# Kernel tuning notes

Hardware: AMD Instinct MI355X
Metric: run time of the kernel (lower is better)

The kernel has to match this reference:

```python
import jax, jax.numpy as jnp
import numpy as np

B, N, C, H = 1, 1024, 384, 12
DK, DV, P, PV = 16, 16, 4, 4  # scalar key/value dims, query/value points
POINT_KEY_DIM = 4

def setup_inputs() -> dict:
    key = jax.random.key(0)
    ks = jax.random.split(key, 12)
    s = 0.02
    x = jax.random.normal(ks[0], (B, N, C), dtype=jnp.float32)
    # random orthonormal frames via QR
    A = jax.random.normal(ks[1], (B, N, 3, 3), dtype=jnp.float32)
    rotations, _ = jnp.linalg.qr(A)
    translations = jax.random.normal(ks[2], (B, N, 3), dtype=jnp.float32) * 10.0
    Wq  = jax.random.normal(ks[3], (C, H * DK), dtype=jnp.float32) * s
    Wk  = jax.random.normal(ks[4], (C, H * DK), dtype=jnp.float32) * s
    Wv  = jax.random.normal(ks[5], (C, H * DV), dtype=jnp.float32) * s
    Wqp = jax.random.normal(ks[6], (C, H * P * 3), dtype=jnp.float32) * s
    Wkp = jax.random.normal(ks[7], (C, H * P * 3), dtype=jnp.float32) * s
    Wvp = jax.random.normal(ks[8], (C, H * PV * 3), dtype=jnp.float32) * s
    Wout = jax.random.normal(ks[9], (H * DV + H * PV, C), dtype=jnp.float32) * s
    bout = jnp.zeros((C,), dtype=jnp.float32)
    return {"x": x, "rotations": rotations, "translations": translations,
            "Wq": Wq, "Wk": Wk, "Wv": Wv, "Wqp": Wqp, "Wkp": Wkp, "Wvp": Wvp,
            "Wout": Wout, "bout": bout}

def reference(x, rotations, translations, Wq, Wk, Wv, Wqp, Wkp, Wvp, Wout, bout):
    b, n, c = x.shape
    h = H
    # scalar q/k/v: (b,n,h,d)
    qs = (x @ Wq).reshape(b, n, h, DK)
    ks_ = (x @ Wk).reshape(b, n, h, DK)
    vs = (x @ Wv).reshape(b, n, h, DV)
    # local points: (b,n,h,p,3)
    qp = (x @ Wqp).reshape(b, n, h, P, 3)
    kp = (x @ Wkp).reshape(b, n, h, P, 3)
    vp = (x @ Wvp).reshape(b, n, h, PV, 3)
    t = translations[:, :, None, None, :]
    # rotate to global frame
    qpg = jnp.einsum('bnij,bnhpj->bnhpi', rotations, qp) + t
    kpg = jnp.einsum('bnij,bnhpj->bnhpi', rotations, kp) + t
    vpg = jnp.einsum('bnij,bnhpj->bnhpi', rotations, vp) + t
    # scalar attention logits (b,h,i,j)
    attn_scalar = jnp.einsum('bihd,bjhd->bhij', qs, ks_)
    # squared distances summed over points and coords, expanded to avoid (n,n,h,p,3) diff tensor
    q2 = (qpg ** 2).sum((-1, -2))          # (b,n,h)
    k2 = (kpg ** 2).sum((-1, -2))          # (b,n,h)
    qk = jnp.einsum('bihpc,bjhpc->bhij', qpg, kpg)
    dist_sq = (q2.transpose(0, 2, 1)[:, :, :, None]
               + k2.transpose(0, 2, 1)[:, :, None, :]
               - 2.0 * qk)                 # (b,h,i,j)
    gamma = np.sqrt(2.0 / (9.0 * POINT_KEY_DIM)).astype(np.float32)
    inv_sqrt_dk = np.float32(1.0 / np.sqrt(DK))
    logits = (attn_scalar - 0.5 * gamma * dist_sq) * inv_sqrt_dk
    w = jax.nn.softmax(logits, axis=-1)    # (b,h,i,j)
    # scalar output: (b,n,h*dv)
    out_scalar = jnp.einsum('bhij,bjhd->bihd', w, vs).reshape(b, n, h * DV)
    # point output in global frame, then back to local frame of residue i
    out_pts_g = jnp.einsum('bhij,bjhpc->bihpc', w, vpg)   # (b,n,h,pv,3)
    centered = out_pts_g - t
    out_pts_local = jnp.einsum('bnji,bnhpj->bnhpi', rotations, centered)
    out_pts_norm = jnp.sqrt((out_pts_local ** 2).sum(-1)).reshape(b, n, h * PV)
    out = jnp.concatenate([out_scalar, out_pts_norm], axis=-1)
    return out @ Wout + bout
```

## Files before the change

kernel.cpp:

```cpp
#include <hip/hip_runtime.h>
#include <math.h>

#define N_TOK 1024
#define C_DIM 384
#define H_NUM 12
#define PCOLS 1024
#define Q0 0
#define K0 192
#define V0 384
#define QP0 576
#define KP0 720
#define VP0 864
#define ATT_W 240
#define COEF 0.11785113019775792f
#define ISD 0.25f
#define CC2 (COEF * ISD)
#define KV_ROWS 60
#define NZ 4

__global__ __launch_bounds__(256) void k_pack(
    const float* __restrict__ Wq, const float* __restrict__ Wk, const float* __restrict__ Wv,
    const float* __restrict__ Wqp, const float* __restrict__ Wkp, const float* __restrict__ Wvp,
    float* __restrict__ Wall)
{
    int t = blockIdx.x * 256 + threadIdx.x;
    int k = t >> 8;
    int col = (t & 255) * 4;
    float4 v;
    if (col < 192)       v = *(const float4*)(Wq  + k * 192 + col);
    else if (col < 384)  v = *(const float4*)(Wk  + k * 192 + col - 192);
    else if (col < 576)  v = *(const float4*)(Wv  + k * 192 + col - 384);
    else if (col < 720)  v = *(const float4*)(Wqp + k * 144 + col - 576);
    else if (col < 864)  v = *(const float4*)(Wkp + k * 144 + col - 720);
    else if (col < 1008) v = *(const float4*)(Wvp + k * 144 + col - 864);
    else                 v = make_float4(0.f, 0.f, 0.f, 0.f);
    *(float4*)(Wall + k * PCOLS + col) = v;
}

__global__ __launch_bounds__(256) void k_proj(
    const float* __restrict__ x, const float* __restrict__ Wall, float* __restrict__ P)
{
    __shared__ float xs[64][17];
    __shared__ float wsh[16][64];
    int tid = threadIdx.x;
    int i0 = blockIdx.x * 64, c0 = blockIdx.y * 64;
    int lr = tid >> 2, lk = (tid & 3) * 4;
    int wr = tid >> 4, wc = (tid & 15) * 4;
    int ty = tid >> 4, tx = tid & 15;

    float4 xa = *(const float4*)(x + (i0 + lr) * C_DIM + lk);
    float4 wa = *(const float4*)(Wall + wr * PCOLS + c0 + wc);
    float acc[4][4] = {};

    for (int it = 0; it < 24; ++it) {
        xs[lr][lk + 0] = xa.x; xs[lr][lk + 1] = xa.y;
        xs[lr][lk + 2] = xa.z; xs[lr][lk + 3] = xa.w;
        *(float4*)&wsh[wr][wc] = wa;
        __syncthreads();
        if (it < 23) {
            xa = *(const float4*)(x + (i0 + lr) * C_DIM + (it + 1) * 16 + lk);
            wa = *(const float4*)(Wall + ((it + 1) * 16 + wr) * PCOLS + c0 + wc);
        }
#pragma unroll
        for (int kk = 0; kk < 16; ++kk) {
            float4 b = *(float4*)&wsh[kk][tx * 4];
            float a0 = xs[ty * 4 + 0][kk];
            float a1 = xs[ty * 4 + 1][kk];
            float a2 = xs[ty * 4 + 2][kk];
            float a3 = xs[ty * 4 + 3][kk];
            acc[0][0] = fmaf(a0, b.x, acc[0][0]); acc[0][1] = fmaf(a0, b.y, acc[0][1]);
            acc[0][2] = fmaf(a0, b.z, acc[0][2]); acc[0][3] = fmaf(a0, b.w, acc[0][3]);
            acc[1][0] = fmaf(a1, b.x, acc[1][0]); acc[1][1] = fmaf(a1, b.y, acc[1][1]);
            acc[1][2] = fmaf(a1, b.z, acc[1][2]); acc[1][3] = fmaf(a1, b.w, acc[1][3]);
            acc[2][0] = fmaf(a2, b.x, acc[2][0]); acc[2][1] = fmaf(a2, b.y, acc[2][1]);
            acc[2][2] = fmaf(a2, b.z, acc[2][2]); acc[2][3] = fmaf(a2, b.w, acc[2][3]);
            acc[3][0] = fmaf(a3, b.x, acc[3][0]); acc[3][1] = fmaf(a3, b.y, acc[3][1]);
            acc[3][2] = fmaf(a3, b.z, acc[3][2]); acc[3][3] = fmaf(a3, b.w, acc[3][3]);
        }
        __syncthreads();
    }
#pragma unroll
    for (int r = 0; r < 4; ++r) {
        *(float4*)(P + (i0 + ty * 4 + r) * PCOLS + c0 + tx * 4) =
            make_float4(acc[r][0], acc[r][1], acc[r][2], acc[r][3]);
    }
}

__global__ __launch_bounds__(256) void k_prep(
    const float* __restrict__ P, const float* __restrict__ rot, const float* __restrict__ trans,
    float* __restrict__ KVg, float* __restrict__ Qg, float* __restrict__ qcg)
{
    __shared__ float kb[29 * 128];
    __shared__ float qb[29 * 128];
    __shared__ float vb[28 * 128];
    __shared__ float qcb[128];
    int h = blockIdx.y, nb = blockIdx.x;
    int tid = threadIdx.x;
    int nl = tid & 127, role = tid >> 7;
    int n = nb * 128 + nl;
    const float* R = rot + n * 9;
    float R00 = R[0], R01 = R[1], R02 = R[2];
    float R10 = R[3], R11 = R[4], R12 = R[5];
    float R20 = R[6], R21 = R[7], R22 = R[8];
    float t0 = trans[n * 3 + 0], t1 = trans[n * 3 + 1], t2 = trans[n * 3 + 2];

    if (role == 0) {
        const float* kr = P + n * PCOLS + K0 + h * 16;
#pragma unroll
        for (int d = 0; d < 16; ++d) kb[d * 128 + nl] = kr[d];
        const float* kp = P + n * PCOLS + KP0 + h * 12;
        float k2 = 0.f;
#pragma unroll
        for (int pt = 0; pt < 4; ++pt) {
            float p0 = kp[pt * 3 + 0], p1 = kp[pt * 3 + 1], p2 = kp[pt * 3 + 2];
            float g0 = R00 * p0 + R01 * p1 + R02 * p2 + t0;
            float g1 = R10 * p0 + R11 * p1 + R12 * p2 + t1;
            float g2 = R20 * p0 + R21 * p1 + R22 * p2 + t2;
            kb[(16 + pt * 3 + 0) * 128 + nl] = g0;
            kb[(16 + pt * 3 + 1) * 128 + nl] = g1;
            kb[(16 + pt * 3 + 2) * 128 + nl] = g2;
            k2 += g0 * g0 + g1 * g1 + g2 * g2;
        }
        kb[28 * 128 + nl] = -CC2 * k2;
    } else {
        const float* qr = P + n * PCOLS + Q0 + h * 16;
#pragma unroll
        for (int d = 0; d < 16; ++d) qb[d * 128 + nl] = qr[d] * ISD;
        const float* qp = P + n * PCOLS + QP0 + h * 12;
        float q2 = 0.f;
#pragma unroll
        for (int pt = 0; pt < 4; ++pt) {
            float p0 = qp[pt * 3 + 0], p1 = qp[pt * 3 + 1], p2 = qp[pt * 3 + 2];
            float g0 = R00 * p0 + R01 * p1 + R02 * p2 + t0;
            float g1 = R10 * p0 + R11 * p1 + R12 * p2 + t1;
            float g2 = R20 * p0 + R21 * p1 + R22 * p2 + t2;
            qb[(16 + pt * 3 + 0) * 128 + nl] = g0 * (2.f * CC2);
            qb[(16 + pt * 3 + 1) * 128 + nl] = g1 * (2.f * CC2);
            qb[(16 + pt * 3 + 2) * 128 + nl] = g2 * (2.f * CC2);
            q2 += g0 * g0 + g1 * g1 + g2 * g2;
        }
        qb[28 * 128 + nl] = 1.0f;
        qcb[nl] = fmaf(-CC2, q2, -4.0f);
        const float* vr = P + n * PCOLS + V0 + h * 16;
#pragma unroll
        for (int d = 0; d < 16; ++d) vb[d * 128 + nl] = vr[d];
        const float* vp = P + n * PCOLS + VP0 + h * 12;
#pragma unroll
        for (int pt = 0; pt < 4; ++pt) {
            float p0 = vp[pt * 3 + 0], p1 = vp[pt * 3 + 1], p2 = vp[pt * 3 + 2];
            vb[(16 + pt * 3 + 0) * 128 + nl] = R00 * p0 + R01 * p1 + R02 * p2 + t0;
            vb[(16 + pt * 3 + 1) * 128 + nl] = R10 * p0 + R11 * p1 + R12 * p2 + t1;
            vb[(16 + pt * 3 + 2) * 128 + nl] = R20 * p0 + R21 * p1 + R22 * p2 + t2;
        }
    }
    __syncthreads();

    for (int u = tid; u < 57 * 32; u += 256) {
        int d = u >> 5, c4 = u & 31;
        float4 v = (d < 29) ? *(float4*)&kb[d * 128 + c4 * 4]
                            : *(float4*)&vb[(d - 29) * 128 + c4 * 4];
        *(float4*)&KVg[(h * KV_ROWS + d) * 1024 + nb * 128 + c4 * 4] = v;
    }
    for (int u = tid; u < 29 * 32; u += 256) {
        int d = u >> 5, c4 = u & 31;
        *(float4*)&Qg[(h * 29 + d) * 1024 + nb * 128 + c4 * 4] = *(float4*)&qb[d * 128 + c4 * 4];
    }
    if (tid < 32) *(float4*)&qcg[h * 1024 + nb * 128 + tid * 4] = *(float4*)&qcb[tid * 4];
}

__global__ __launch_bounds__(256, 3) void k_attn(
    const float* __restrict__ KVg, const float* __restrict__ Qg,
    const float* __restrict__ qcg, float* __restrict__ part)
{
    __shared__ float Qs[29 * 64];
    __shared__ float KV[2][KV_ROWS * 64];
    int tid = threadIdx.x;
    int lane = tid & 63, w = tid >> 6;
    int ty = tid >> 3, tx = tid & 7;

    int bid = blockIdx.x;
    int xcd = bid & 7, slot = bid >> 3;
    int pair = xcd * 6 + (slot >> 4);
    int bx = slot & 15;
    int h = pair % H_NUM;
    int z = pair / H_NUM;

    int i0 = bx * 64;
    int jz0 = z * 256;
    const float* KVh = KVg + h * KV_ROWS * 1024;

    for (int u = tid; u < 29 * 16; u += 256) {
        int d = u >> 4, c4 = u & 15;
        *(float4*)&Qs[d * 64 + c4 * 4] = *(const float4*)&Qg[(h * 29 + d) * 1024 + i0 + c4 * 4];
    }
    float qc[2];
#pragma unroll
    for (int r = 0; r < 2; ++r) qc[r] = qcg[h * 1024 + i0 + ty * 2 + r];

    int nst = (w < 3) ? 4 : 3;
#define STAGE(T) do { float* buf_ = KV[(T) & 1]; int j0_ = jz0 + (T) * 64;        \
        for (int m_ = 0; m_ < nst; ++m_) {                                        \
            int g_ = w * 4 + m_;                                                  \
            const float* src_ = KVh + (g_ * 4 + (lane >> 4)) * 1024 + j0_ + (lane & 15) * 4; \
            float* dst_ = buf_ + g_ * 256;                                        \
            __builtin_amdgcn_global_load_lds(                                     \
                (const __attribute__((address_space(1))) void*)src_,              \
                (__attribute__((address_space(3))) void*)dst_, 16, 0, 0);         \
        } } while (0)

    STAGE(0);
    __syncthreads();

    float out[2][28] = {};
    float denom[2] = {};

    for (int t = 0; t < 4; ++t) {
        if (t < 3) STAGE(t + 1);
        const float* Kb = KV[t & 1];
        const float* Vb = Kb + 29 * 64;

        float s[2][8] = {};
#pragma unroll
        for (int d = 0; d < 29; ++d) {
            float2 qv = *(const float2*)&Qs[d * 64 + ty * 2];
            float4 k0 = *(const float4*)&Kb[d * 64 + tx * 8];
            float4 k1 = *(const float4*)&Kb[d * 64 + tx * 8 + 4];
            float ka[8] = {k0.x, k0.y, k0.z, k0.w, k1.x, k1.y, k1.z, k1.w};
#pragma unroll
            for (int j = 0; j < 8; ++j) {
                s[0][j] = fmaf(qv.x, ka[j], s[0][j]);
                s[1][j] = fmaf(qv.y, ka[j], s[1][j]);
            }
        }

        float p[2][8];
#pragma unroll
        for (int r = 0; r < 2; ++r) {
#pragma unroll
            for (int j = 0; j < 8; ++j) {
                p[r][j] = __expf(s[r][j] + qc[r]);
                denom[r] += p[r][j];
            }
        }

#pragma unroll
        for (int d = 0; d < 28; ++d) {
            float4 v0 = *(const float4*)&Vb[d * 64 + tx * 8];
            float4 v1 = *(const float4*)&Vb[d * 64 + tx * 8 + 4];
            float va[8] = {v0.x, v0.y, v0.z, v0.w, v1.x, v1.y, v1.z, v1.w};
#pragma unroll
            for (int r = 0; r < 2; ++r) {
                float acc = out[r][d];
#pragma unroll
                for (int j = 0; j < 8; ++j) acc = fmaf(p[r][j], va[j], acc);
                out[r][d] = acc;
            }
        }
        __syncthreads();
    }

#pragma unroll
    for (int m = 1; m <= 4; m <<= 1) {
#pragma unroll
        for (int r = 0; r < 2; ++r) {
#pragma unroll
            for (int d = 0; d < 28; ++d) out[r][d] += __shfl_xor(out[r][d], m, 64);
            denom[r] += __shfl_xor(denom[r], m, 64);
        }
    }
    if (tx == 0) {
#pragma unroll
        for (int r = 0; r < 2; ++r) {
#pragma unroll
            for (int d = 0; d < 28; ++d) Qs[d * 64 + ty * 2 + r] = out[r][d];
            Qs[28 * 64 + ty * 2 + r] = denom[r];
        }
    }
    __syncthreads();
    for (int u = tid; u < 29 * 64; u += 256) {
        part[((z * H_NUM + h) * 29 + (u >> 6)) * N_TOK + i0 + (u & 63)] = Qs[u];
    }
}

__global__ __launch_bounds__(256) void k_comb(
    const float* __restrict__ part, const float* __restrict__ rot,
    const float* __restrict__ trans, float* __restrict__ att)
{
    int t = blockIdx.x * 256 + threadIdx.x;
    int h = t >> 10, i = t & 1023;
    float v[29];
#pragma unroll
    for (int c = 0; c < 29; ++c) {
        float s = 0.f;
#pragma unroll
        for (int z = 0; z < NZ; ++z)
            s += part[((z * H_NUM + h) * 29 + c) * N_TOK + i];
        v[c] = s;
    }
    float inv = 1.f / v[28];
    float* arow = att + i * ATT_W;
#pragma unroll
    for (int d = 0; d < 16; ++d) arow[h * 16 + d] = v[d] * inv;
    float t0 = trans[i * 3 + 0], t1 = trans[i * 3 + 1], t2v = trans[i * 3 + 2];
    const float* R = rot + i * 9;
#pragma unroll
    for (int p = 0; p < 4; ++p) {
        float c0 = v[16 + p * 3 + 0] * inv - t0;
        float c1 = v[16 + p * 3 + 1] * inv - t1;
        float c2 = v[16 + p * 3 + 2] * inv - t2v;
        float l0 = R[0] * c0 + R[3] * c1 + R[6] * c2;
        float l1 = R[1] * c0 + R[4] * c1 + R[7] * c2;
        float l2 = R[2] * c0 + R[5] * c1 + R[8] * c2;
        arow[192 + h * 4 + p] = sqrtf(l0 * l0 + l1 * l1 + l2 * l2);
    }
}

__global__ __launch_bounds__(256) void k_out(
    const float* __restrict__ att, const float* __restrict__ Wout,
    const float* __restrict__ bout, float* __restrict__ out)
{
    __shared__ float xs[64][17];
    __shared__ float wsh[16][64];
    int tid = threadIdx.x;
    int i0 = blockIdx.x * 64, c0 = blockIdx.y * 64;
    int lr = tid >> 2, lk = (tid & 3) * 4;
    int wr = tid >> 4, wc = (tid & 15) * 4;
    int ty = tid >> 4, tx = tid & 15;

    float4 xa = *(const float4*)(att + (i0 + lr) * ATT_W + lk);
    float4 wa = *(const float4*)(Wout + wr * C_DIM + c0 + wc);
    float acc[4][4] = {};

    for (int it = 0; it < 15; ++it) {
        xs[lr][lk + 0] = xa.x; xs[lr][lk + 1] = xa.y;
        xs[lr][lk + 2] = xa.z; xs[lr][lk + 3] = xa.w;
        *(float4*)&wsh[wr][wc] = wa;
        __syncthreads();
        if (it < 14) {
            xa = *(const float4*)(att + (i0 + lr) * ATT_W + (it + 1) * 16 + lk);
            wa = *(const float4*)(Wout + ((it + 1) * 16 + wr) * C_DIM + c0 + wc);
        }
#pragma unroll
        for (int kk = 0; kk < 16; ++kk) {
            float4 b = *(float4*)&wsh[kk][tx * 4];
            float a0 = xs[ty * 4 + 0][kk];
            float a1 = xs[ty * 4 + 1][kk];
            float a2 = xs[ty * 4 + 2][kk];
            float a3 = xs[ty * 4 + 3][kk];
            acc[0][0] = fmaf(a0, b.x, acc[0][0]); acc[0][1] = fmaf(a0, b.y, acc[0][1]);
            acc[0][2] = fmaf(a0, b.z, acc[0][2]); acc[0][3] = fmaf(a0, b.w, acc[0][3]);
            acc[1][0] = fmaf(a1, b.x, acc[1][0]); acc[1][1] = fmaf(a1, b.y, acc[1][1]);
            acc[1][2] = fmaf(a1, b.z, acc[1][2]); acc[1][3] = fmaf(a1, b.w, acc[1][3]);
            acc[2][0] = fmaf(a2, b.x, acc[2][0]); acc[2][1] = fmaf(a2, b.y, acc[2][1]);
            acc[2][2] = fmaf(a2, b.z, acc[2][2]); acc[2][3] = fmaf(a2, b.w, acc[2][3]);
            acc[3][0] = fmaf(a3, b.x, acc[3][0]); acc[3][1] = fmaf(a3, b.y, acc[3][1]);
            acc[3][2] = fmaf(a3, b.z, acc[3][2]); acc[3][3] = fmaf(a3, b.w, acc[3][3]);
        }
        __syncthreads();
    }
    float4 bb = *(const float4*)(bout + c0 + tx * 4);
#pragma unroll
    for (int r = 0; r < 4; ++r) {
        *(float4*)(out + (i0 + ty * 4 + r) * C_DIM + c0 + tx * 4) =
            make_float4(acc[r][0] + bb.x, acc[r][1] + bb.y, acc[r][2] + bb.z, acc[r][3] + bb.w);
    }
}

extern "C" void kernel_launch(void* const* d_in, const int* in_sizes, int n_in,
                              void* d_out, int out_size, void* d_ws, size_t ws_size,
                              hipStream_t stream) {
    const float* x     = (const float*)d_in[0];
    const float* rot   = (const float*)d_in[1];
    const float* trans = (const float*)d_in[2];
    const float* Wq    = (const float*)d_in[3];
    const float* Wk    = (const float*)d_in[4];
    const float* Wv    = (const float*)d_in[5];
    const float* Wqp   = (const float*)d_in[6];
    const float* Wkp   = (const float*)d_in[7];
    const float* Wvp   = (const float*)d_in[8];
    const float* Wout  = (const float*)d_in[9];
    const float* bout  = (const float*)d_in[10];
    float* out = (float*)d_out;

    float* ws = (float*)d_ws;
    float* Wall = ws;
    float* P    = Wall + C_DIM * PCOLS;
    float* KVg  = P    + N_TOK * PCOLS;
    float* Qg   = KVg  + H_NUM * KV_ROWS * 1024;
    float* qcg  = Qg   + H_NUM * 29 * 1024;
    float* part = ws;
    float* att  = Qg;

    k_pack<<<384, 256, 0, stream>>>(Wq, Wk, Wv, Wqp, Wkp, Wvp, Wall);
    k_proj<<<dim3(16, 16), 256, 0, stream>>>(x, Wall, P);
    k_prep<<<dim3(8, 12), 256, 0, stream>>>(P, rot, trans, KVg, Qg, qcg);
    k_attn<<<768, 256, 0, stream>>>(KVg, Qg, qcg, part);
    k_comb<<<48, 256, 0, stream>>>(part, rot, trans, att);
    k_out<<<dim3(16, 6), 256, 0, stream>>>(att, Wout, bout, out);
}
```

Before: 94.05 us.

## Replace LDS-tiled projection GEMMs with register-only double-buffered global loads

Both small GEMMs (input projection and output projection) stop staging tiles in shared memory. Each thread now loads its own x/att rows and weight columns straight from global memory into registers, double-buffered so the next slice's loads overlap the current FMAs, and no barriers are needed. The output GEMM also shrinks to 1x4 outputs per thread with four times as many blocks to improve occupancy. The trade-off is losing the shared-memory reuse across the block, so redundant global and L2 traffic rises, and the caches must absorb the repeated weight reads.

```diff
diff --git a/kernel.cpp b/kernel.cpp
--- a/kernel.cpp
+++ b/kernel.cpp
@@ -37,53 +37,55 @@
     *(float4*)(Wall + k * PCOLS + col) = v;
 }
 
-__global__ __launch_bounds__(256) void k_proj(
+__global__ __launch_bounds__(256, 1) void k_proj(
     const float* __restrict__ x, const float* __restrict__ Wall, float* __restrict__ P)
 {
-    __shared__ float xs[64][17];
-    __shared__ float wsh[16][64];
     int tid = threadIdx.x;
-    int i0 = blockIdx.x * 64, c0 = blockIdx.y * 64;
-    int lr = tid >> 2, lk = (tid & 3) * 4;
-    int wr = tid >> 4, wc = (tid & 15) * 4;
     int ty = tid >> 4, tx = tid & 15;
-
-    float4 xa = *(const float4*)(x + (i0 + lr) * C_DIM + lk);
-    float4 wa = *(const float4*)(Wall + wr * PCOLS + c0 + wc);
+    int row0 = blockIdx.x * 64 + ty * 4;
+    int col0 = blockIdx.y * 64 + tx * 4;
+    const float* xr = x + row0 * C_DIM;
+    const float* wp = Wall + col0;
+
     float acc[4][4] = {};
-
-    for (int it = 0; it < 24; ++it) {
-        xs[lr][lk + 0] = xa.x; xs[lr][lk + 1] = xa.y;
-        xs[lr][lk + 2] = xa.z; xs[lr][lk + 3] = xa.w;
-        *(float4*)&wsh[wr][wc] = wa;
-        __syncthreads();
-        if (it < 23) {
-            xa = *(const float4*)(x + (i0 + lr) * C_DIM + (it + 1) * 16 + lk);
-            wa = *(const float4*)(Wall + ((it + 1) * 16 + wr) * PCOLS + c0 + wc);
-        }
-#pragma unroll
-        for (int kk = 0; kk < 16; ++kk) {
-            float4 b = *(float4*)&wsh[kk][tx * 4];
-            float a0 = xs[ty * 4 + 0][kk];
-            float a1 = xs[ty * 4 + 1][kk];
-            float a2 = xs[ty * 4 + 2][kk];
-            float a3 = xs[ty * 4 + 3][kk];
-            acc[0][0] = fmaf(a0, b.x, acc[0][0]); acc[0][1] = fmaf(a0, b.y, acc[0][1]);
-            acc[0][2] = fmaf(a0, b.z, acc[0][2]); acc[0][3] = fmaf(a0, b.w, acc[0][3]);
-            acc[1][0] = fmaf(a1, b.x, acc[1][0]); acc[1][1] = fmaf(a1, b.y, acc[1][1]);
-            acc[1][2] = fmaf(a1, b.z, acc[1][2]); acc[1][3] = fmaf(a1, b.w, acc[1][3]);
-            acc[2][0] = fmaf(a2, b.x, acc[2][0]); acc[2][1] = fmaf(a2, b.y, acc[2][1]);
-            acc[2][2] = fmaf(a2, b.z, acc[2][2]); acc[2][3] = fmaf(a2, b.w, acc[2][3]);
-            acc[3][0] = fmaf(a3, b.x, acc[3][0]); acc[3][1] = fmaf(a3, b.y, acc[3][1]);
-            acc[3][2] = fmaf(a3, b.z, acc[3][2]); acc[3][3] = fmaf(a3, b.w, acc[3][3]);
-        }
-        __syncthreads();
-    }
-#pragma unroll
-    for (int r = 0; r < 4; ++r) {
-        *(float4*)(P + (i0 + ty * 4 + r) * PCOLS + c0 + tx * 4) =
+    float A[4][4], B[4][4], An[4][4], Bn[4][4];
+
+#pragma unroll
+    for (int r = 0; r < 4; ++r) *(float4*)A[r] = *(const float4*)(xr + r * C_DIM);
+#pragma unroll
+    for (int u = 0; u < 4; ++u) *(float4*)B[u] = *(const float4*)(wp + u * PCOLS);
+
+#define PROJ_FMA(AA, BB)                                                      \
+    _Pragma("unroll")                                                         \
+    for (int u = 0; u < 4; ++u) {                                             \
+        _Pragma("unroll")                                                     \
+        for (int r = 0; r < 4; ++r) {                                         \
+            _Pragma("unroll")                                                 \
+            for (int c = 0; c < 4; ++c)                                       \
+                acc[r][c] = fmaf(AA[r][u], BB[u][c], acc[r][c]);              \
+        }                                                                     \
+    }
+
+    for (int q = 0; q < 96; q += 2) {
+        int k1 = (q + 1) * 4;
+#pragma unroll
+        for (int r = 0; r < 4; ++r) *(float4*)An[r] = *(const float4*)(xr + r * C_DIM + k1);
+#pragma unroll
+        for (int u = 0; u < 4; ++u) *(float4*)Bn[u] = *(const float4*)(wp + (k1 + u) * PCOLS);
+        PROJ_FMA(A, B);
+        if (q + 2 < 96) {
+            int k2 = (q + 2) * 4;
+#pragma unroll
+            for (int r = 0; r < 4; ++r) *(float4*)A[r] = *(const float4*)(xr + r * C_DIM + k2);
+#pragma unroll
+            for (int u = 0; u < 4; ++u) *(float4*)B[u] = *(const float4*)(wp + (k2 + u) * PCOLS);
+        }
+        PROJ_FMA(An, Bn);
+    }
+#pragma unroll
+    for (int r = 0; r < 4; ++r)
+        *(float4*)(P + (row0 + r) * PCOLS + col0) =
             make_float4(acc[r][0], acc[r][1], acc[r][2], acc[r][3]);
-    }
 }
 
 __global__ __launch_bounds__(256) void k_prep(
@@ -315,55 +317,49 @@
     }
 }
 
-__global__ __launch_bounds__(256) void k_out(
+__global__ __launch_bounds__(256, 1) void k_out(
     const float* __restrict__ att, const float* __restrict__ Wout,
     const float* __restrict__ bout, float* __restrict__ out)
 {
-    __shared__ float xs[64][17];
-    __shared__ float wsh[16][64];
     int tid = threadIdx.x;
-    int i0 = blockIdx.x * 64, c0 = blockIdx.y * 64;
-    int lr = tid >> 2, lk = (tid & 3) * 4;
-    int wr = tid >> 4, wc = (tid & 15) * 4;
     int ty = tid >> 4, tx = tid & 15;
-
-    float4 xa = *(const float4*)(att + (i0 + lr) * ATT_W + lk);
-    float4 wa = *(const float4*)(Wout + wr * C_DIM + c0 + wc);
-    float acc[4][4] = {};
-
-    for (int it = 0; it < 15; ++it) {
-        xs[lr][lk + 0] = xa.x; xs[lr][lk + 1] = xa.y;
-        xs[lr][lk + 2] = xa.z; xs[lr][lk + 3] = xa.w;
-        *(float4*)&wsh[wr][wc] = wa;
-        __syncthreads();
-        if (it < 14) {
-            xa = *(const float4*)(att + (i0 + lr) * ATT_W + (it + 1) * 16 + lk);
-            wa = *(const float4*)(Wout + ((it + 1) * 16 + wr) * C_DIM + c0 + wc);
-        }
-#pragma unroll
-        for (int kk = 0; kk < 16; ++kk) {
-            float4 b = *(float4*)&wsh[kk][tx * 4];
-            float a0 = xs[ty * 4 + 0][kk];
-            float a1 = xs[ty * 4 + 1][kk];
-            float a2 = xs[ty * 4 + 2][kk];
-            float a3 = xs[ty * 4 + 3][kk];
-            acc[0][0] = fmaf(a0, b.x, acc[0][0]); acc[0][1] = fmaf(a0, b.y, acc[0][1]);
-            acc[0][2] = fmaf(a0, b.z, acc[0][2]); acc[0][3] = fmaf(a0, b.w, acc[0][3]);
-            acc[1][0] = fmaf(a1, b.x, acc[1][0]); acc[1][1] = fmaf(a1, b.y, acc[1][1]);
-            acc[1][2] = fmaf(a1, b.z, acc[1][2]); acc[1][3] = fmaf(a1, b.w, acc[1][3]);
-            acc[2][0] = fmaf(a2, b.x, acc[2][0]); acc[2][1] = fmaf(a2, b.y, acc[2][1]);
-            acc[2][2] = fmaf(a2, b.z, acc[2][2]); acc[2][3] = fmaf(a2, b.w, acc[2][3]);
-            acc[3][0] = fmaf(a3, b.x, acc[3][0]); acc[3][1] = fmaf(a3, b.y, acc[3][1]);
-            acc[3][2] = fmaf(a3, b.z, acc[3][2]); acc[3][3] = fmaf(a3, b.w, acc[3][3]);
-        }
-        __syncthreads();
-    }
-    float4 bb = *(const float4*)(bout + c0 + tx * 4);
-#pragma unroll
-    for (int r = 0; r < 4; ++r) {
-        *(float4*)(out + (i0 + ty * 4 + r) * C_DIM + c0 + tx * 4) =
-            make_float4(acc[r][0] + bb.x, acc[r][1] + bb.y, acc[r][2] + bb.z, acc[r][3] + bb.w);
-    }
+    int row = blockIdx.x * 16 + ty;
+    int col0 = blockIdx.y * 64 + tx * 4;
+    const float* ar = att + row * ATT_W;
+    const float* wp = Wout + col0;
+
+    float acc[4] = {};
+    float A[4], B[4][4], An[4], Bn[4][4];
+
+    *(float4*)A = *(const float4*)ar;
+#pragma unroll
+    for (int u = 0; u < 4; ++u) *(float4*)B[u] = *(const float4*)(wp + u * C_DIM);
+
+#define OUT_FMA(AA, BB)                                                       \
+    _Pragma("unroll")                                                         \
+    for (int u = 0; u < 4; ++u) {                                             \
+        _Pragma("unroll")                                                     \
+        for (int c = 0; c < 4; ++c)                                           \
+            acc[c] = fmaf(AA[u], BB[u][c], acc[c]);                           \
+    }
+
+    for (int q = 0; q < 60; q += 2) {
+        int k1 = (q + 1) * 4;
+        *(float4*)An = *(const float4*)(ar + k1);
+#pragma unroll
+        for (int u = 0; u < 4; ++u) *(float4*)Bn[u] = *(const float4*)(wp + (k1 + u) * C_DIM);
+        OUT_FMA(A, B);
+        if (q + 2 < 60) {
+            int k2 = (q + 2) * 4;
+            *(float4*)A = *(const float4*)(ar + k2);
+#pragma unroll
+            for (int u = 0; u < 4; ++u) *(float4*)B[u] = *(const float4*)(wp + (k2 + u) * C_DIM);
+        }
+        OUT_FMA(An, Bn);
+    }
+    float4 bb = *(const float4*)(bout + col0);
+    *(float4*)(out + row * C_DIM + col0) =
+        make_float4(acc[0] + bb.x, acc[1] + bb.y, acc[2] + bb.z, acc[3] + bb.w);
 }
 
 extern "C" void kernel_launch(void* const* d_in, const int* in_sizes, int n_in,
@@ -396,5 +392,5 @@
     k_prep<<<dim3(8, 12), 256, 0, stream>>>(P, rot, trans, KVg, Qg, qcg);
     k_attn<<<768, 256, 0, stream>>>(KVg, Qg, qcg, part);
     k_comb<<<48, 256, 0, stream>>>(part, rot, trans, att);
-    k_out<<<dim3(16, 6), 256, 0, stream>>>(att, Wout, bout, out);
-}
+    k_out<<<dim3(64, 6), 256, 0, stream>>>(att, Wout, bout, out);
+}
```

Result: slower. 108.2 us (+15.0%).

## Load GEMM A operands directly into registers and double-buffer weight tiles

Applied to the files above, without the earlier changes.

Both the projection and output GEMMs now read their A operands straight from global memory into registers as float4 vectors instead of staging them in shared memory. The weight tile is double-buffered in shared memory, so each iteration needs one barrier instead of two. The output GEMM shrinks to 32-row tiles with 2 rows per thread, doubling the block count to fill more compute units. The cost is more global/L2 traffic for A, since threads sharing rows load them redundantly, and higher register use.

```diff
diff --git a/kernel.cpp b/kernel.cpp
--- a/kernel.cpp
+++ b/kernel.cpp
@@ -40,50 +40,55 @@
 __global__ __launch_bounds__(256) void k_proj(
     const float* __restrict__ x, const float* __restrict__ Wall, float* __restrict__ P)
 {
-    __shared__ float xs[64][17];
-    __shared__ float wsh[16][64];
+    __shared__ float wsh[2][16][64];
     int tid = threadIdx.x;
-    int i0 = blockIdx.x * 64, c0 = blockIdx.y * 64;
-    int lr = tid >> 2, lk = (tid & 3) * 4;
+    int ty = tid >> 4, tx = tid & 15;
     int wr = tid >> 4, wc = (tid & 15) * 4;
-    int ty = tid >> 4, tx = tid & 15;
-
-    float4 xa = *(const float4*)(x + (i0 + lr) * C_DIM + lk);
-    float4 wa = *(const float4*)(Wall + wr * PCOLS + c0 + wc);
+    int row0 = blockIdx.x * 64 + ty * 4;
+    int col0 = blockIdx.y * 64;
+    const float* xr = x + row0 * C_DIM;
+
     float acc[4][4] = {};
+    {
+        float4 w0 = *(const float4*)(Wall + wr * PCOLS + col0 + wc);
+        *(float4*)&wsh[0][wr][wc] = w0;
+    }
+    __syncthreads();
 
     for (int it = 0; it < 24; ++it) {
-        xs[lr][lk + 0] = xa.x; xs[lr][lk + 1] = xa.y;
-        xs[lr][lk + 2] = xa.z; xs[lr][lk + 3] = xa.w;
-        *(float4*)&wsh[wr][wc] = wa;
+        float4 Ar[4][4];
+#pragma unroll
+        for (int r = 0; r < 4; ++r)
+#pragma unroll
+            for (int q = 0; q < 4; ++q)
+                Ar[r][q] = *(const float4*)(xr + r * C_DIM + it * 16 + q * 4);
+        if (it < 23) {
+            float4 wn = *(const float4*)(Wall + ((it + 1) * 16 + wr) * PCOLS + col0 + wc);
+            *(float4*)&wsh[(it + 1) & 1][wr][wc] = wn;
+        }
+        const float (*wb)[64] = wsh[it & 1];
+#pragma unroll
+        for (int q = 0; q < 4; ++q) {
+#pragma unroll
+            for (int u = 0; u < 4; ++u) {
+                float4 b = *(const float4*)&wb[q * 4 + u][tx * 4];
+#pragma unroll
+                for (int r = 0; r < 4; ++r) {
+                    float a = (u == 0) ? Ar[r][q].x : (u == 1) ? Ar[r][q].y
+                             : (u == 2) ? Ar[r][q].z : Ar[r][q].w;
+                    acc[r][0] = fmaf(a, b.x, acc[r][0]);
+                    acc[r][1] = fmaf(a, b.y, acc[r][1]);
+                    acc[r][2] = fmaf(a, b.z, acc[r][2]);
+                    acc[r][3] = fmaf(a, b.w, acc[r][3]);
+                }
+            }
+        }
         __syncthreads();
-        if (it < 23) {
-            xa = *(const float4*)(x + (i0 + lr) * C_DIM + (it + 1) * 16 + lk);
-            wa = *(const float4*)(Wall + ((it + 1) * 16 + wr) * PCOLS + c0 + wc);
-        }
-#pragma unroll
-        for (int kk = 0; kk < 16; ++kk) {
-            float4 b = *(float4*)&wsh[kk][tx * 4];
-            float a0 = xs[ty * 4 + 0][kk];
-            float a1 = xs[ty * 4 + 1][kk];
-            float a2 = xs[ty * 4 + 2][kk];
-            float a3 = xs[ty * 4 + 3][kk];
-            acc[0][0] = fmaf(a0, b.x, acc[0][0]); acc[0][1] = fmaf(a0, b.y, acc[0][1]);
-            acc[0][2] = fmaf(a0, b.z, acc[0][2]); acc[0][3] = fmaf(a0, b.w, acc[0][3]);
-            acc[1][0] = fmaf(a1, b.x, acc[1][0]); acc[1][1] = fmaf(a1, b.y, acc[1][1]);
-            acc[1][2] = fmaf(a1, b.z, acc[1][2]); acc[1][3] = fmaf(a1, b.w, acc[1][3]);
-            acc[2][0] = fmaf(a2, b.x, acc[2][0]); acc[2][1] = fmaf(a2, b.y, acc[2][1]);
-            acc[2][2] = fmaf(a2, b.z, acc[2][2]); acc[2][3] = fmaf(a2, b.w, acc[2][3]);
-            acc[3][0] = fmaf(a3, b.x, acc[3][0]); acc[3][1] = fmaf(a3, b.y, acc[3][1]);
-            acc[3][2] = fmaf(a3, b.z, acc[3][2]); acc[3][3] = fmaf(a3, b.w, acc[3][3]);
-        }
-        __syncthreads();
-    }
-#pragma unroll
-    for (int r = 0; r < 4; ++r) {
-        *(float4*)(P + (i0 + ty * 4 + r) * PCOLS + c0 + tx * 4) =
+    }
+#pragma unroll
+    for (int r = 0; r < 4; ++r)
+        *(float4*)(P + (row0 + r) * PCOLS + col0 + tx * 4) =
             make_float4(acc[r][0], acc[r][1], acc[r][2], acc[r][3]);
-    }
 }
 
 __global__ __launch_bounds__(256) void k_prep(
@@ -319,51 +324,56 @@
     const float* __restrict__ att, const float* __restrict__ Wout,
     const float* __restrict__ bout, float* __restrict__ out)
 {
-    __shared__ float xs[64][17];
-    __shared__ float wsh[16][64];
+    __shared__ float wsh[2][16][64];
     int tid = threadIdx.x;
-    int i0 = blockIdx.x * 64, c0 = blockIdx.y * 64;
-    int lr = tid >> 2, lk = (tid & 3) * 4;
+    int ty = tid >> 4, tx = tid & 15;
     int wr = tid >> 4, wc = (tid & 15) * 4;
-    int ty = tid >> 4, tx = tid & 15;
-
-    float4 xa = *(const float4*)(att + (i0 + lr) * ATT_W + lk);
-    float4 wa = *(const float4*)(Wout + wr * C_DIM + c0 + wc);
-    float acc[4][4] = {};
+    int row0 = blockIdx.x * 32 + ty * 2;
+    int col0 = blockIdx.y * 64;
+    const float* ar = att + row0 * ATT_W;
+
+    float acc[2][4] = {};
+    {
+        float4 w0 = *(const float4*)(Wout + wr * C_DIM + col0 + wc);
+        *(float4*)&wsh[0][wr][wc] = w0;
+    }
+    __syncthreads();
 
     for (int it = 0; it < 15; ++it) {
-        xs[lr][lk + 0] = xa.x; xs[lr][lk + 1] = xa.y;
-        xs[lr][lk + 2] = xa.z; xs[lr][lk + 3] = xa.w;
-        *(float4*)&wsh[wr][wc] = wa;
+        float4 Ar[2][4];
+#pragma unroll
+        for (int r = 0; r < 2; ++r)
+#pragma unroll
+            for (int q = 0; q < 4; ++q)
+                Ar[r][q] = *(const float4*)(ar + r * ATT_W + it * 16 + q * 4);
+        if (it < 14) {
+            float4 wn = *(const float4*)(Wout + ((it + 1) * 16 + wr) * C_DIM + col0 + wc);
+            *(float4*)&wsh[(it + 1) & 1][wr][wc] = wn;
+        }
+        const float (*wb)[64] = wsh[it & 1];
+#pragma unroll
+        for (int q = 0; q < 4; ++q) {
+#pragma unroll
+            for (int u = 0; u < 4; ++u) {
+                float4 b = *(const float4*)&wb[q * 4 + u][tx * 4];
+#pragma unroll
+                for (int r = 0; r < 2; ++r) {
+                    float a = (u == 0) ? Ar[r][q].x : (u == 1) ? Ar[r][q].y
+                             : (u == 2) ? Ar[r][q].z : Ar[r][q].w;
+                    acc[r][0] = fmaf(a, b.x, acc[r][0]);
+                    acc[r][1] = fmaf(a, b.y, acc[r][1]);
+                    acc[r][2] = fmaf(a, b.z, acc[r][2]);
+                    acc[r][3] = fmaf(a, b.w, acc[r][3]);
+                }
+            }
+        }
         __syncthreads();
-        if (it < 14) {
-            xa = *(const float4*)(att + (i0 + lr) * ATT_W + (it + 1) * 16 + lk);
-            wa = *(const float4*)(Wout + ((it + 1) * 16 + wr) * C_DIM + c0 + wc);
-        }
-#pragma unroll
-        for (int kk = 0; kk < 16; ++kk) {
-            float4 b = *(float4*)&wsh[kk][tx * 4];
-            float a0 = xs[ty * 4 + 0][kk];
-            float a1 = xs[ty * 4 + 1][kk];
-            float a2 = xs[ty * 4 + 2][kk];
-            float a3 = xs[ty * 4 + 3][kk];
-            acc[0][0] = fmaf(a0, b.x, acc[0][0]); acc[0][1] = fmaf(a0, b.y, acc[0][1]);
-            acc[0][2] = fmaf(a0, b.z, acc[0][2]); acc[0][3] = fmaf(a0, b.w, acc[0][3]);
-            acc[1][0] = fmaf(a1, b.x, acc[1][0]); acc[1][1] = fmaf(a1, b.y, acc[1][1]);
-            acc[1][2] = fmaf(a1, b.z, acc[1][2]); acc[1][3] = fmaf(a1, b.w, acc[1][3]);
-            acc[2][0] = fmaf(a2, b.x, acc[2][0]); acc[2][1] = fmaf(a2, b.y, acc[2][1]);
-            acc[2][2] = fmaf(a2, b.z, acc[2][2]); acc[2][3] = fmaf(a2, b.w, acc[2][3]);
-            acc[3][0] = fmaf(a3, b.x, acc[3][0]); acc[3][1] = fmaf(a3, b.y, acc[3][1]);
-            acc[3][2] = fmaf(a3, b.z, acc[3][2]); acc[3][3] = fmaf(a3, b.w, acc[3][3]);
-        }
-        __syncthreads();
-    }
-    float4 bb = *(const float4*)(bout + c0 + tx * 4);
-#pragma unroll
-    for (int r = 0; r < 4; ++r) {
-        *(float4*)(out + (i0 + ty * 4 + r) * C_DIM + c0 + tx * 4) =
+    }
+    float4 bb = *(const float4*)(bout + col0 + tx * 4);
+#pragma unroll
+    for (int r = 0; r < 2; ++r)
+        *(float4*)(out + (row0 + r) * C_DIM + col0 + tx * 4) =
             make_float4(acc[r][0] + bb.x, acc[r][1] + bb.y, acc[r][2] + bb.z, acc[r][3] + bb.w);
-    }
 }
 
 extern "C" void kernel_launch(void* const* d_in, const int* in_sizes, int n_in,
@@ -396,5 +406,5 @@
     k_prep<<<dim3(8, 12), 256, 0, stream>>>(P, rot, trans, KVg, Qg, qcg);
     k_attn<<<768, 256, 0, stream>>>(KVg, Qg, qcg, part);
     k_comb<<<48, 256, 0, stream>>>(part, rot, trans, att);
-    k_out<<<dim3(16, 6), 256, 0, stream>>>(att, Wout, bout, out);
-}
+    k_out<<<dim3(32, 6), 256, 0, stream>>>(att, Wout, bout, out);
+}
```

After: 100.2 us. +6.6%, slower.

## Fuse weight packing into projection GEMM and keep attention queries in registers

Applied to the files above, without the earlier changes.

Removes the separate weight-packing kernel: the projection GEMM now reads directly from the six weight matrices, choosing a base pointer per 64-column tile. The x tile in shared memory is transposed so each thread reads four rows with one float4 load. In the attention kernel, each thread's 29x2 query values are held in registers instead of being read from shared memory on every iteration, and the launch-bounds occupancy hint drops from 3 to 2 blocks to make room for the extra registers. Workspace buffers are laid out separately instead of aliasing. This saves a launch and a global round-trip, at the risk of lower occupancy in the attention kernel.

```diff
diff --git a/kernel.cpp b/kernel.cpp
--- a/kernel.cpp
+++ b/kernel.cpp
@@ -18,29 +18,13 @@
 #define KV_ROWS 60
 #define NZ 4
 
-__global__ __launch_bounds__(256) void k_pack(
+__global__ __launch_bounds__(256) void k_proj(
+    const float* __restrict__ x,
     const float* __restrict__ Wq, const float* __restrict__ Wk, const float* __restrict__ Wv,
     const float* __restrict__ Wqp, const float* __restrict__ Wkp, const float* __restrict__ Wvp,
-    float* __restrict__ Wall)
-{
-    int t = blockIdx.x * 256 + threadIdx.x;
-    int k = t >> 8;
-    int col = (t & 255) * 4;
-    float4 v;
-    if (col < 192)       v = *(const float4*)(Wq  + k * 192 + col);
-    else if (col < 384)  v = *(const float4*)(Wk  + k * 192 + col - 192);
-    else if (col < 576)  v = *(const float4*)(Wv  + k * 192 + col - 384);
-    else if (col < 720)  v = *(const float4*)(Wqp + k * 144 + col - 576);
-    else if (col < 864)  v = *(const float4*)(Wkp + k * 144 + col - 720);
-    else if (col < 1008) v = *(const float4*)(Wvp + k * 144 + col - 864);
-    else                 v = make_float4(0.f, 0.f, 0.f, 0.f);
-    *(float4*)(Wall + k * PCOLS + col) = v;
-}
-
-__global__ __launch_bounds__(256) void k_proj(
-    const float* __restrict__ x, const float* __restrict__ Wall, float* __restrict__ P)
-{
-    __shared__ float xs[64][17];
+    float* __restrict__ P)
+{
+    __shared__ float xs[16][68];
     __shared__ float wsh[16][64];
     int tid = threadIdx.x;
     int i0 = blockIdx.x * 64, c0 = blockIdx.y * 64;
@@ -48,42 +32,49 @@
     int wr = tid >> 4, wc = (tid & 15) * 4;
     int ty = tid >> 4, tx = tid & 15;
 
+    int col = c0 + wc;
+    const float* Wb; int od, cb;
+    if (col < 192)       { Wb = Wq;  od = 192; cb = col; }
+    else if (col < 384)  { Wb = Wk;  od = 192; cb = col - 192; }
+    else if (col < 576)  { Wb = Wv;  od = 192; cb = col - 384; }
+    else if (col < 720)  { Wb = Wqp; od = 144; cb = col - 576; }
+    else if (col < 864)  { Wb = Wkp; od = 144; cb = col - 720; }
+    else if (col < 1008) { Wb = Wvp; od = 144; cb = col - 864; }
+    else                 { Wb = nullptr; od = 0; cb = 0; }
+
     float4 xa = *(const float4*)(x + (i0 + lr) * C_DIM + lk);
-    float4 wa = *(const float4*)(Wall + wr * PCOLS + c0 + wc);
+    float4 wa = Wb ? *(const float4*)(Wb + wr * od + cb) : make_float4(0.f, 0.f, 0.f, 0.f);
     float acc[4][4] = {};
 
     for (int it = 0; it < 24; ++it) {
-        xs[lr][lk + 0] = xa.x; xs[lr][lk + 1] = xa.y;
-        xs[lr][lk + 2] = xa.z; xs[lr][lk + 3] = xa.w;
+        xs[lk + 0][lr] = xa.x; xs[lk + 1][lr] = xa.y;
+        xs[lk + 2][lr] = xa.z; xs[lk + 3][lr] = xa.w;
         *(float4*)&wsh[wr][wc] = wa;
         __syncthreads();
         if (it < 23) {
             xa = *(const float4*)(x + (i0 + lr) * C_DIM + (it + 1) * 16 + lk);
-            wa = *(const float4*)(Wall + ((it + 1) * 16 + wr) * PCOLS + c0 + wc);
+            wa = Wb ? *(const float4*)(Wb + ((it + 1) * 16 + wr) * od + cb)
+                    : make_float4(0.f, 0.f, 0.f, 0.f);
         }
 #pragma unroll
         for (int kk = 0; kk < 16; ++kk) {
+            float4 a = *(float4*)&xs[kk][ty * 4];
             float4 b = *(float4*)&wsh[kk][tx * 4];
-            float a0 = xs[ty * 4 + 0][kk];
-            float a1 = xs[ty * 4 + 1][kk];
-            float a2 = xs[ty * 4 + 2][kk];
-            float a3 = xs[ty * 4 + 3][kk];
-            acc[0][0] = fmaf(a0, b.x, acc[0][0]); acc[0][1] = fmaf(a0, b.y, acc[0][1]);
-            acc[0][2] = fmaf(a0, b.z, acc[0][2]); acc[0][3] = fmaf(a0, b.w, acc[0][3]);
-            acc[1][0] = fmaf(a1, b.x, acc[1][0]); acc[1][1] = fmaf(a1, b.y, acc[1][1]);
-            acc[1][2] = fmaf(a1, b.z, acc[1][2]); acc[1][3] = fmaf(a1, b.w, acc[1][3]);
-            acc[2][0] = fmaf(a2, b.x, acc[2][0]); acc[2][1] = fmaf(a2, b.y, acc[2][1]);
-            acc[2][2] = fmaf(a2, b.z, acc[2][2]); acc[2][3] = fmaf(a2, b.w, acc[2][3]);
-            acc[3][0] = fmaf(a3, b.x, acc[3][0]); acc[3][1] = fmaf(a3, b.y, acc[3][1]);
-            acc[3][2] = fmaf(a3, b.z, acc[3][2]); acc[3][3] = fmaf(a3, b.w, acc[3][3]);
-        }
-        __syncthreads();
-    }
-#pragma unroll
-    for (int r = 0; r < 4; ++r) {
+            acc[0][0] = fmaf(a.x, b.x, acc[0][0]); acc[0][1] = fmaf(a.x, b.y, acc[0][1]);
+            acc[0][2] = fmaf(a.x, b.z, acc[0][2]); acc[0][3] = fmaf(a.x, b.w, acc[0][3]);
+            acc[1][0] = fmaf(a.y, b.x, acc[1][0]); acc[1][1] = fmaf(a.y, b.y, acc[1][1]);
+            acc[1][2] = fmaf(a.y, b.z, acc[1][2]); acc[1][3] = fmaf(a.y, b.w, acc[1][3]);
+            acc[2][0] = fmaf(a.z, b.x, acc[2][0]); acc[2][1] = fmaf(a.z, b.y, acc[2][1]);
+            acc[2][2] = fmaf(a.z, b.z, acc[2][2]); acc[2][3] = fmaf(a.z, b.w, acc[2][3]);
+            acc[3][0] = fmaf(a.w, b.x, acc[3][0]); acc[3][1] = fmaf(a.w, b.y, acc[3][1]);
+            acc[3][2] = fmaf(a.w, b.z, acc[3][2]); acc[3][3] = fmaf(a.w, b.w, acc[3][3]);
+        }
+        __syncthreads();
+    }
+#pragma unroll
+    for (int r = 0; r < 4; ++r)
         *(float4*)(P + (i0 + ty * 4 + r) * PCOLS + c0 + tx * 4) =
             make_float4(acc[r][0], acc[r][1], acc[r][2], acc[r][3]);
-    }
 }
 
 __global__ __launch_bounds__(256) void k_prep(
@@ -168,12 +159,12 @@
     if (tid < 32) *(float4*)&qcg[h * 1024 + nb * 128 + tid * 4] = *(float4*)&qcb[tid * 4];
 }
 
-__global__ __launch_bounds__(256, 3) void k_attn(
+__global__ __launch_bounds__(256, 2) void k_attn(
     const float* __restrict__ KVg, const float* __restrict__ Qg,
     const float* __restrict__ qcg, float* __restrict__ part)
 {
-    __shared__ float Qs[29 * 64];
     __shared__ float KV[2][KV_ROWS * 64];
+    __shared__ float red[29 * 64];
     int tid = threadIdx.x;
     int lane = tid & 63, w = tid >> 6;
     int ty = tid >> 3, tx = tid & 7;
@@ -189,13 +180,17 @@
     int jz0 = z * 256;
     const float* KVh = KVg + h * KV_ROWS * 1024;
 
-    for (int u = tid; u < 29 * 16; u += 256) {
-        int d = u >> 4, c4 = u & 15;
-        *(float4*)&Qs[d * 64 + c4 * 4] = *(const float4*)&Qg[(h * 29 + d) * 1024 + i0 + c4 * 4];
+    float q0[29], q1[29];
+#pragma unroll
+    for (int d = 0; d < 29; ++d) {
+        float2 qv = *(const float2*)&Qg[(h * 29 + d) * 1024 + i0 + ty * 2];
+        q0[d] = qv.x; q1[d] = qv.y;
     }
     float qc[2];
-#pragma unroll
-    for (int r = 0; r < 2; ++r) qc[r] = qcg[h * 1024 + i0 + ty * 2 + r];
+    {
+        float2 qcv = *(const float2*)&qcg[h * 1024 + i0 + ty * 2];
+        qc[0] = qcv.x; qc[1] = qcv.y;
+    }
 
     int nst = (w < 3) ? 4 : 3;
 #define STAGE(T) do { float* buf_ = KV[(T) & 1]; int j0_ = jz0 + (T) * 64;        \
@@ -222,14 +217,13 @@
         float s[2][8] = {};
 #pragma unroll
         for (int d = 0; d < 29; ++d) {
-            float2 qv = *(const float2*)&Qs[d * 64 + ty * 2];
             float4 k0 = *(const float4*)&Kb[d * 64 + tx * 8];
             float4 k1 = *(const float4*)&Kb[d * 64 + tx * 8 + 4];
             float ka[8] = {k0.x, k0.y, k0.z, k0.w, k1.x, k1.y, k1.z, k1.w};
 #pragma unroll
             for (int j = 0; j < 8; ++j) {
-                s[0][j] = fmaf(qv.x, ka[j], s[0][j]);
-                s[1][j] = fmaf(qv.y, ka[j], s[1][j]);
+                s[0][j] = fmaf(q0[d], ka[j], s[0][j]);
+                s[1][j] = fmaf(q1[d], ka[j], s[1][j]);
             }
         }
 
@@ -272,13 +266,13 @@
 #pragma unroll
         for (int r = 0; r < 2; ++r) {
 #pragma unroll
-            for (int d = 0; d < 28; ++d) Qs[d * 64 + ty * 2 + r] = out[r][d];
-            Qs[28 * 64 + ty * 2 + r] = denom[r];
+            for (int d = 0; d < 28; ++d) red[d * 64 + ty * 2 + r] = out[r][d];
+            red[28 * 64 + ty * 2 + r] = denom[r];
         }
     }
     __syncthreads();
     for (int u = tid; u < 29 * 64; u += 256) {
-        part[((z * H_NUM + h) * 29 + (u >> 6)) * N_TOK + i0 + (u & 63)] = Qs[u];
+        part[((z * H_NUM + h) * 29 + (u >> 6)) * N_TOK + i0 + (u & 63)] = red[u];
     }
 }
 
@@ -382,17 +376,15 @@
     const float* bout  = (const float*)d_in[10];
     float* out = (float*)d_out;
 
-    float* ws = (float*)d_ws;
-    float* Wall = ws;
-    float* P    = Wall + C_DIM * PCOLS;
+    float* ws  = (float*)d_ws;
+    float* P    = ws;
     float* KVg  = P    + N_TOK * PCOLS;
     float* Qg   = KVg  + H_NUM * KV_ROWS * 1024;
     float* qcg  = Qg   + H_NUM * 29 * 1024;
-    float* part = ws;
-    float* att  = Qg;
-
-    k_pack<<<384, 256, 0, stream>>>(Wq, Wk, Wv, Wqp, Wkp, Wvp, Wall);
-    k_proj<<<dim3(16, 16), 256, 0, stream>>>(x, Wall, P);
+    float* part = qcg  + H_NUM * 1024;
+    float* att  = part + NZ * H_NUM * 29 * 1024;
+
+    k_proj<<<dim3(16, 16), 256, 0, stream>>>(x, Wq, Wk, Wv, Wqp, Wkp, Wvp, P);
     k_prep<<<dim3(8, 12), 256, 0, stream>>>(P, rot, trans, KVg, Qg, qcg);
     k_attn<<<768, 256, 0, stream>>>(KVg, Qg, qcg, part);
     k_comb<<<48, 256, 0, stream>>>(part, rot, trans, att);
```

Result: faster. 85.61 us (-9.0%).
